# Performance work log

Hardware: AMD Instinct MI355X
Metric: run time of the kernel (lower is better)

The kernel has to match this reference:

```python
import jax, jax.numpy as jnp
import numpy as np

S = 30.0
ML = 0.4
MS = 0.1
N, D, C = 8192, 1024, 10240

def setup_inputs() -> dict:
    key = jax.random.key(0)
    k1, k2, k3 = jax.random.split(key, 3)
    x = jax.random.normal(k1, (N, D), dtype=jnp.float32)
    labels = jax.random.randint(k2, (N,), 0, C, dtype=jnp.int64)
    # xavier_uniform for weight (C, D)
    limit = float(np.sqrt(6.0 / (C + D)))
    weight = jax.random.uniform(k3, (C, D), dtype=jnp.float32, minval=-limit, maxval=limit)
    return {"x": x, "labels": labels, "weight": weight}

def _l2norm(v, axis):
    # matches F.normalize (eps=1e-12)
    n = jnp.sqrt(jnp.sum(v * v, axis=axis, keepdims=True))
    return v / jnp.maximum(n, 1e-12)

def reference(x, labels, weight):
    # cosine logits, clamped to [-1, 1]
    wf = jnp.clip(_l2norm(x, 1) @ _l2norm(weight, 1).T, -1.0, 1.0)  # (N, C)
    # per-sample additive margin: ml if label<=5 (real) else ms (fake)
    m = jnp.where(labels <= 5, ML, MS).astype(wf.dtype)  # (N,)
    target = jnp.take_along_axis(wf, labels[:, None], axis=1)[:, 0]  # wf[i, labels[i]]
    numerator = S * (target - m)
    # sum over j != label of exp(s*wf[i,j]) == full sum minus the label term
    exp_all = jnp.exp(S * wf)
    excl_sum = jnp.sum(exp_all, axis=1) - jnp.exp(S * target)
    denominator = jnp.exp(numerator) + excl_sum
    L = numerator - jnp.log(denominator)
    return -jnp.mean(L)
```

## Files before the change

### kernel.cpp

```cpp
#include <hip/hip_runtime.h>
#include <hip/hip_bf16.h>

#define N_ROWS 8192
#define DIM    1024
#define NCLS   10240
#define S_SCALE 30.0f
#define M_LARGE 0.4f
#define M_SMALL 0.1f

typedef __attribute__((ext_vector_type(4))) int   i32x4;

#define GLD16(gp, lp) __builtin_amdgcn_global_load_lds( \
    (const __attribute__((address_space(1))) unsigned int*)(gp), \
    (__attribute__((address_space(3))) unsigned int*)(lp), 16, 0, 0)

__global__ void prep_kernel(const float* __restrict__ x, const float* __restrict__ w,
                            float* __restrict__ inv_x, float* __restrict__ inv_w,
                            float* __restrict__ fx, float* __restrict__ fw,
                            float* __restrict__ gsum,
                            signed char* __restrict__ xq, signed char* __restrict__ wq){
    int b = blockIdx.x;
    bool isx = (b < N_ROWS);
    int r = isx ? b : b - N_ROWS;
    const float4* src = (const float4*)((isx ? x : w) + (size_t)r * DIM);
    float4 v = src[threadIdx.x];
    float ss = v.x*v.x + v.y*v.y + v.z*v.z + v.w*v.w;
    float am = fmaxf(fmaxf(fabsf(v.x), fabsf(v.y)), fmaxf(fabsf(v.z), fabsf(v.w)));
    #pragma unroll
    for (int o = 32; o; o >>= 1){
        ss += __shfl_down(ss, o);
        am  = fmaxf(am, __shfl_down(am, o));
    }
    __shared__ float pss[4], pam[4];
    int lane = threadIdx.x & 63, wid = threadIdx.x >> 6;
    if (lane == 0){ pss[wid] = ss; pam[wid] = am; }
    __syncthreads();
    float t    = pss[0] + pss[1] + pss[2] + pss[3];
    float amax = fmaxf(fmaxf(pam[0], pam[1]), fmaxf(pam[2], pam[3]));
    float inv  = 1.0f / fmaxf(sqrtf(t), 1e-12f);
    float s    = fmaxf(amax, 1e-20f) * (1.0f/127.0f);
    float rs   = 127.0f / fmaxf(amax, 1e-20f);
    int q0 = __float2int_rn(v.x * rs), q1 = __float2int_rn(v.y * rs);
    int q2 = __float2int_rn(v.z * rs), q3 = __float2int_rn(v.w * rs);
    unsigned int pk = (q0 & 0xff) | ((q1 & 0xff) << 8) | ((q2 & 0xff) << 16) | ((q3 & 0xff) << 24);
    ((unsigned int*)((isx ? xq : wq) + (size_t)r * DIM))[threadIdx.x] = pk;
    if (threadIdx.x == 0){
        if (isx){ inv_x[r] = inv; fx[r] = s * inv; gsum[r] = 0.0f; }
        else    { inv_w[r] = inv; fw[r] = s * inv; }
    }
}

__global__ void target_kernel(const float* __restrict__ x, const float* __restrict__ w,
                              const int* __restrict__ labels,
                              const float* __restrict__ inv_x, const float* __restrict__ inv_w,
                              float* __restrict__ tgt){
    int wid = threadIdx.x >> 6, lane = threadIdx.x & 63;
    int i = blockIdx.x * 4 + wid;
    int lab = labels[i];
    const float4* xp = (const float4*)(x + (size_t)i   * DIM);
    const float4* wp = (const float4*)(w + (size_t)lab * DIM);
    float acc = 0.f;
    #pragma unroll
    for (int c = 0; c < 4; ++c){
        float4 a = xp[c*64 + lane];
        float4 b = wp[c*64 + lane];
        acc += a.x*b.x + a.y*b.y + a.z*b.z + a.w*b.w;
    }
    #pragma unroll
    for (int o = 32; o; o >>= 1) acc += __shfl_down(acc, o);
    if (lane == 0){
        float c = acc * inv_x[i] * inv_w[lab];
        c = fminf(fmaxf(c, -1.f), 1.f);
        tgt[i] = c;
    }
}

#define BM 256
#define BN 256
#define BKB 128
#define NT (DIM/BKB)
#define GRID_X (NCLS/BN)
#define GRID_Y (N_ROWS/BM)
#define NWG (GRID_X*GRID_Y)

__global__ __launch_bounds__(512, 2) void gemm_kernel(
        const signed char* __restrict__ xq, const signed char* __restrict__ wq,
        const float* __restrict__ fx, const float* __restrict__ fw,
        float* __restrict__ gsum){
    __shared__ __align__(16) unsigned char As[2][BM*BKB];
    __shared__ __align__(16) unsigned char Bs[2][BN*BKB];
    __shared__ float sumrow[BM];

    int tid = threadIdx.x;
    int bid = blockIdx.x;
    int swz = (bid & 7) * (NWG/8) + (bid >> 3);
    int by = swz / GRID_X, bx = swz % GRID_X;
    int row0 = by * BM, col0 = bx * BN;
    int wid = tid >> 6, lane = tid & 63;
    int wm = wid >> 2, wn = wid & 3;
    int g = lane >> 4, l16 = lane & 15;

    if (tid < BM) sumrow[tid] = 0.f;

    int srow = tid >> 3;
    int csrc = (tid & 7) ^ (srow & 7);
    const signed char* gA = xq + (size_t)(row0 + srow) * DIM + csrc * 16;
    const signed char* gB = wq + (size_t)(col0 + srow) * DIM + csrc * 16;
    int ldso = srow * BKB + (tid & 7) * 16;

    i32x4 acc[8][4] = {};

    #pragma unroll
    for (int h = 0; h < 4; ++h){
        GLD16(gA + (size_t)(h*64)*DIM, &As[0][h*64*BKB + ldso]);
        GLD16(gB + (size_t)(h*64)*DIM, &Bs[0][h*64*BKB + ldso]);
    }
    __syncthreads();

    for (int kt = 0; kt < NT; ++kt){
        int b = kt & 1, nb = b ^ 1;
        int knext = (kt + 1) * BKB;
        bool pre = (kt + 1 < NT);

        if (pre){
            GLD16(gA + knext,                    &As[nb][ldso]);
            GLD16(gA + knext + (size_t)64*DIM,   &As[nb][64*BKB + ldso]);
            GLD16(gA + knext + (size_t)128*DIM,  &As[nb][128*BKB + ldso]);
            GLD16(gA + knext + (size_t)192*DIM,  &As[nb][192*BKB + ldso]);
        }

        i32x4 af0[8], bf0[4];
        #pragma unroll
        for (int m = 0; m < 8; ++m){
            int r = wm*128 + m*16 + l16;
            af0[m] = *(const i32x4*)&As[b][r*BKB + ((g ^ (r & 7)) << 4)];
        }
        #pragma unroll
        for (int n = 0; n < 4; ++n){
            int r = wn*64 + n*16 + l16;
            bf0[n] = *(const i32x4*)&Bs[b][r*BKB + ((g ^ (r & 7)) << 4)];
        }
        #pragma unroll
        for (int m = 0; m < 8; ++m)
            #pragma unroll
            for (int n = 0; n < 4; ++n)
                acc[m][n] = __builtin_amdgcn_mfma_i32_16x16x64_i8(af0[m], bf0[n], acc[m][n], 0, 0, 0);

        if (pre){
            GLD16(gB + knext,                    &Bs[nb][ldso]);
            GLD16(gB + knext + (size_t)64*DIM,   &Bs[nb][64*BKB + ldso]);
            GLD16(gB + knext + (size_t)128*DIM,  &Bs[nb][128*BKB + ldso]);
            GLD16(gB + knext + (size_t)192*DIM,  &Bs[nb][192*BKB + ldso]);
        }

        i32x4 af1[8], bf1[4];
        #pragma unroll
        for (int m = 0; m < 8; ++m){
            int r = wm*128 + m*16 + l16;
            af1[m] = *(const i32x4*)&As[b][r*BKB + (((4+g) ^ (r & 7)) << 4)];
        }
        #pragma unroll
        for (int n = 0; n < 4; ++n){
            int r = wn*64 + n*16 + l16;
            bf1[n] = *(const i32x4*)&Bs[b][r*BKB + (((4+g) ^ (r & 7)) << 4)];
        }
        #pragma unroll
        for (int m = 0; m < 8; ++m)
            #pragma unroll
            for (int n = 0; n < 4; ++n)
                acc[m][n] = __builtin_amdgcn_mfma_i32_16x16x64_i8(af1[m], bf1[n], acc[m][n], 0, 0, 0);

        asm volatile("s_waitcnt vmcnt(0)" ::: "memory");
        __syncthreads();
    }

    float fwv[4];
    #pragma unroll
    for (int n = 0; n < 4; ++n) fwv[n] = fw[col0 + wn*64 + n*16 + l16];
    #pragma unroll
    for (int m = 0; m < 8; ++m){
        #pragma unroll
        for (int rg = 0; rg < 4; ++rg){
            int rl = wm*128 + m*16 + g*4 + rg;
            float fxr = fx[row0 + rl];
            float v = 0.f;
            #pragma unroll
            for (int n = 0; n < 4; ++n){
                float c = (float)acc[m][n][rg] * fxr * fwv[n];
                c = fminf(fmaxf(c, -1.f), 1.f);
                v += __expf(S_SCALE * c);
            }
            v += __shfl_xor(v, 1);
            v += __shfl_xor(v, 2);
            v += __shfl_xor(v, 4);
            v += __shfl_xor(v, 8);
            if (l16 == 0) atomicAdd(&sumrow[rl], v);
        }
    }
    __syncthreads();
    if (tid < BM) atomicAdd(&gsum[row0 + tid], sumrow[tid]);
}

__global__ void finalize_kernel(const float* __restrict__ tgt, const float* __restrict__ gsum,
                                const int* __restrict__ labels, float* __restrict__ out){
    double local = 0.0;
    for (int i = threadIdx.x; i < N_ROWS; i += 1024){
        float tv = tgt[i];
        float m  = (labels[i] <= 5) ? M_LARGE : M_SMALL;
        float numer = S_SCALE * (tv - m);
        float excl  = gsum[i] - __expf(S_SCALE * tv);
        float denom = __expf(numer) + excl;
        float L = numer - logf(denom);
        local += (double)L;
    }
    #pragma unroll
    for (int o = 32; o; o >>= 1) local += __shfl_down(local, o);
    __shared__ double part[16];
    int lane = threadIdx.x & 63, wid = threadIdx.x >> 6;
    if (lane == 0) part[wid] = local;
    __syncthreads();
    if (threadIdx.x == 0){
        double s = 0.0;
        #pragma unroll
        for (int p = 0; p < 16; ++p) s += part[p];
        out[0] = (float)(-s / (double)N_ROWS);
    }
}

extern "C" void kernel_launch(void* const* d_in, const int* in_sizes, int n_in,
                              void* d_out, int out_size, void* d_ws, size_t ws_size,
                              hipStream_t stream) {
    const float* x      = (const float*)d_in[0];
    const int*   labels = (const int*)  d_in[1];
    const float* w      = (const float*)d_in[2];

    float* ws    = (float*)d_ws;
    float* inv_x = ws;
    float* inv_w = inv_x + N_ROWS;
    float* fx    = inv_w + NCLS;
    float* fw    = fx    + N_ROWS;
    float* tgt   = fw    + NCLS;
    float* gsum  = tgt   + N_ROWS;
    signed char* xq = (signed char*)(gsum + N_ROWS);
    signed char* wq = xq + (size_t)N_ROWS * DIM;

    prep_kernel<<<N_ROWS + NCLS, 256, 0, stream>>>(x, w, inv_x, inv_w, fx, fw, gsum, xq, wq);
    target_kernel<<<N_ROWS/4, 256, 0, stream>>>(x, w, labels, inv_x, inv_w, tgt);
    gemm_kernel<<<NWG, 512, 0, stream>>>(xq, wq, fx, fw, gsum);
    finalize_kernel<<<1, 1024, 0, stream>>>(tgt, gsum, labels, (float*)d_out);
}
```

Baseline: 156.5 us.

## Fuse target-logit extraction into int8 GEMM epilogue and shrink tiles to 128x128

Removes the separate fp32 target_kernel and instead has the GEMM epilogue write the clamped cosine for each row's label column into tgt, using labels staged in shared memory. The target logit now comes from the int8-quantized product rather than the exact fp32 dot product, which changes accuracy. The GEMM tile also shrinks from 256x256 with 512 threads to 128x128 with 256 threads, and prefetch is issued all at once before compute. This saves a launch and a full reread of x and w rows, but halves per-tile data reuse and doubles global traffic for the quantized operands.

```diff
diff --git a/kernel.cpp b/kernel.cpp
--- a/kernel.cpp
+++ b/kernel.cpp
@@ -15,7 +15,6 @@
     (__attribute__((address_space(3))) unsigned int*)(lp), 16, 0, 0)
 
 __global__ void prep_kernel(const float* __restrict__ x, const float* __restrict__ w,
-                            float* __restrict__ inv_x, float* __restrict__ inv_w,
                             float* __restrict__ fx, float* __restrict__ fw,
                             float* __restrict__ gsum,
                             signed char* __restrict__ xq, signed char* __restrict__ wq){
@@ -45,51 +44,28 @@
     unsigned int pk = (q0 & 0xff) | ((q1 & 0xff) << 8) | ((q2 & 0xff) << 16) | ((q3 & 0xff) << 24);
     ((unsigned int*)((isx ? xq : wq) + (size_t)r * DIM))[threadIdx.x] = pk;
     if (threadIdx.x == 0){
-        if (isx){ inv_x[r] = inv; fx[r] = s * inv; gsum[r] = 0.0f; }
-        else    { inv_w[r] = inv; fw[r] = s * inv; }
-    }
-}
-
-__global__ void target_kernel(const float* __restrict__ x, const float* __restrict__ w,
-                              const int* __restrict__ labels,
-                              const float* __restrict__ inv_x, const float* __restrict__ inv_w,
-                              float* __restrict__ tgt){
-    int wid = threadIdx.x >> 6, lane = threadIdx.x & 63;
-    int i = blockIdx.x * 4 + wid;
-    int lab = labels[i];
-    const float4* xp = (const float4*)(x + (size_t)i   * DIM);
-    const float4* wp = (const float4*)(w + (size_t)lab * DIM);
-    float acc = 0.f;
-    #pragma unroll
-    for (int c = 0; c < 4; ++c){
-        float4 a = xp[c*64 + lane];
-        float4 b = wp[c*64 + lane];
-        acc += a.x*b.x + a.y*b.y + a.z*b.z + a.w*b.w;
-    }
-    #pragma unroll
-    for (int o = 32; o; o >>= 1) acc += __shfl_down(acc, o);
-    if (lane == 0){
-        float c = acc * inv_x[i] * inv_w[lab];
-        c = fminf(fmaxf(c, -1.f), 1.f);
-        tgt[i] = c;
-    }
-}
-
-#define BM 256
-#define BN 256
+        if (isx){ fx[r] = s * inv; gsum[r] = 0.0f; }
+        else      fw[r] = s * inv;
+    }
+}
+
+#define BM 128
+#define BN 128
 #define BKB 128
 #define NT (DIM/BKB)
 #define GRID_X (NCLS/BN)
 #define GRID_Y (N_ROWS/BM)
 #define NWG (GRID_X*GRID_Y)
 
-__global__ __launch_bounds__(512, 2) void gemm_kernel(
+__global__ __launch_bounds__(256, 2) void gemm_kernel(
         const signed char* __restrict__ xq, const signed char* __restrict__ wq,
         const float* __restrict__ fx, const float* __restrict__ fw,
-        float* __restrict__ gsum){
+        const int* __restrict__ labels,
+        float* __restrict__ gsum, float* __restrict__ tgt){
     __shared__ __align__(16) unsigned char As[2][BM*BKB];
     __shared__ __align__(16) unsigned char Bs[2][BN*BKB];
     __shared__ float sumrow[BM];
+    __shared__ int   lab_s[BM];
 
     int tid = threadIdx.x;
     int bid = blockIdx.x;
@@ -97,10 +73,10 @@
     int by = swz / GRID_X, bx = swz % GRID_X;
     int row0 = by * BM, col0 = bx * BN;
     int wid = tid >> 6, lane = tid & 63;
-    int wm = wid >> 2, wn = wid & 3;
+    int wm = wid >> 1, wn = wid & 1;
     int g = lane >> 4, l16 = lane & 15;
 
-    if (tid < BM) sumrow[tid] = 0.f;
+    if (tid < BM){ sumrow[tid] = 0.f; lab_s[tid] = labels[row0 + tid]; }
 
     int srow = tid >> 3;
     int csrc = (tid & 7) ^ (srow & 7);
@@ -108,67 +84,45 @@
     const signed char* gB = wq + (size_t)(col0 + srow) * DIM + csrc * 16;
     int ldso = srow * BKB + (tid & 7) * 16;
 
-    i32x4 acc[8][4] = {};
+    i32x4 acc[4][4] = {};
 
     #pragma unroll
     for (int h = 0; h < 4; ++h){
-        GLD16(gA + (size_t)(h*64)*DIM, &As[0][h*64*BKB + ldso]);
-        GLD16(gB + (size_t)(h*64)*DIM, &Bs[0][h*64*BKB + ldso]);
+        GLD16(gA + (size_t)(h*32)*DIM, &As[0][h*32*BKB + ldso]);
+        GLD16(gB + (size_t)(h*32)*DIM, &Bs[0][h*32*BKB + ldso]);
     }
     __syncthreads();
 
     for (int kt = 0; kt < NT; ++kt){
         int b = kt & 1, nb = b ^ 1;
-        int knext = (kt + 1) * BKB;
-        bool pre = (kt + 1 < NT);
-
-        if (pre){
-            GLD16(gA + knext,                    &As[nb][ldso]);
-            GLD16(gA + knext + (size_t)64*DIM,   &As[nb][64*BKB + ldso]);
-            GLD16(gA + knext + (size_t)128*DIM,  &As[nb][128*BKB + ldso]);
-            GLD16(gA + knext + (size_t)192*DIM,  &As[nb][192*BKB + ldso]);
+        if (kt + 1 < NT){
+            int kn = (kt + 1) * BKB;
+            #pragma unroll
+            for (int h = 0; h < 4; ++h){
+                GLD16(gA + kn + (size_t)(h*32)*DIM, &As[nb][h*32*BKB + ldso]);
+                GLD16(gB + kn + (size_t)(h*32)*DIM, &Bs[nb][h*32*BKB + ldso]);
+            }
         }
 
-        i32x4 af0[8], bf0[4];
         #pragma unroll
-        for (int m = 0; m < 8; ++m){
-            int r = wm*128 + m*16 + l16;
-            af0[m] = *(const i32x4*)&As[b][r*BKB + ((g ^ (r & 7)) << 4)];
+        for (int kk = 0; kk < 2; ++kk){
+            i32x4 af[4], bfv[4];
+            #pragma unroll
+            for (int m = 0; m < 4; ++m){
+                int r = wm*64 + m*16 + l16;
+                af[m] = *(const i32x4*)&As[b][r*BKB + (((kk*4+g) ^ (r & 7)) << 4)];
+            }
+            #pragma unroll
+            for (int n = 0; n < 4; ++n){
+                int r = wn*64 + n*16 + l16;
+                bfv[n] = *(const i32x4*)&Bs[b][r*BKB + (((kk*4+g) ^ (r & 7)) << 4)];
+            }
+            #pragma unroll
+            for (int m = 0; m < 4; ++m)
+                #pragma unroll
+                for (int n = 0; n < 4; ++n)
+                    acc[m][n] = __builtin_amdgcn_mfma_i32_16x16x64_i8(af[m], bfv[n], acc[m][n], 0, 0, 0);
         }
-        #pragma unroll
-        for (int n = 0; n < 4; ++n){
-            int r = wn*64 + n*16 + l16;
-            bf0[n] = *(const i32x4*)&Bs[b][r*BKB + ((g ^ (r & 7)) << 4)];
-        }
-        #pragma unroll
-        for (int m = 0; m < 8; ++m)
-            #pragma unroll
-            for (int n = 0; n < 4; ++n)
-                acc[m][n] = __builtin_amdgcn_mfma_i32_16x16x64_i8(af0[m], bf0[n], acc[m][n], 0, 0, 0);
-
-        if (pre){
-            GLD16(gB + knext,                    &Bs[nb][ldso]);
-            GLD16(gB + knext + (size_t)64*DIM,   &Bs[nb][64*BKB + ldso]);
-            GLD16(gB + knext + (size_t)128*DIM,  &Bs[nb][128*BKB + ldso]);
-            GLD16(gB + knext + (size_t)192*DIM,  &Bs[nb][192*BKB + ldso]);
-        }
-
-        i32x4 af1[8], bf1[4];
-        #pragma unroll
-        for (int m = 0; m < 8; ++m){
-            int r = wm*128 + m*16 + l16;
-            af1[m] = *(const i32x4*)&As[b][r*BKB + (((4+g) ^ (r & 7)) << 4)];
-        }
-        #pragma unroll
-        for (int n = 0; n < 4; ++n){
-            int r = wn*64 + n*16 + l16;
-            bf1[n] = *(const i32x4*)&Bs[b][r*BKB + (((4+g) ^ (r & 7)) << 4)];
-        }
-        #pragma unroll
-        for (int m = 0; m < 8; ++m)
-            #pragma unroll
-            for (int n = 0; n < 4; ++n)
-                acc[m][n] = __builtin_amdgcn_mfma_i32_16x16x64_i8(af1[m], bf1[n], acc[m][n], 0, 0, 0);
 
         asm volatile("s_waitcnt vmcnt(0)" ::: "memory");
         __syncthreads();
@@ -178,17 +132,19 @@
     #pragma unroll
     for (int n = 0; n < 4; ++n) fwv[n] = fw[col0 + wn*64 + n*16 + l16];
     #pragma unroll
-    for (int m = 0; m < 8; ++m){
+    for (int m = 0; m < 4; ++m){
         #pragma unroll
         for (int rg = 0; rg < 4; ++rg){
-            int rl = wm*128 + m*16 + g*4 + rg;
+            int rl = wm*64 + m*16 + g*4 + rg;
             float fxr = fx[row0 + rl];
+            int lab = lab_s[rl];
             float v = 0.f;
             #pragma unroll
             for (int n = 0; n < 4; ++n){
                 float c = (float)acc[m][n][rg] * fxr * fwv[n];
                 c = fminf(fmaxf(c, -1.f), 1.f);
                 v += __expf(S_SCALE * c);
+                if (lab == col0 + wn*64 + n*16 + l16) tgt[row0 + rl] = c;
             }
             v += __shfl_xor(v, 1);
             v += __shfl_xor(v, 2);
@@ -235,17 +191,14 @@
     const float* w      = (const float*)d_in[2];
 
     float* ws    = (float*)d_ws;
-    float* inv_x = ws;
-    float* inv_w = inv_x + N_ROWS;
-    float* fx    = inv_w + NCLS;
+    float* fx    = ws;
     float* fw    = fx    + N_ROWS;
     float* tgt   = fw    + NCLS;
     float* gsum  = tgt   + N_ROWS;
     signed char* xq = (signed char*)(gsum + N_ROWS);
     signed char* wq = xq + (size_t)N_ROWS * DIM;
 
-    prep_kernel<<<N_ROWS + NCLS, 256, 0, stream>>>(x, w, inv_x, inv_w, fx, fw, gsum, xq, wq);
-    target_kernel<<<N_ROWS/4, 256, 0, stream>>>(x, w, labels, inv_x, inv_w, tgt);
-    gemm_kernel<<<NWG, 512, 0, stream>>>(xq, wq, fx, fw, gsum);
+    prep_kernel<<<N_ROWS + NCLS, 256, 0, stream>>>(x, w, fx, fw, gsum, xq, wq);
+    gemm_kernel<<<NWG, 256, 0, stream>>>(xq, wq, fx, fw, labels, gsum, tgt);
     finalize_kernel<<<1, 1024, 0, stream>>>(tgt, gsum, labels, (float*)d_out);
 }
```

Result: slower. 194.1 us (+24.1%).
